# Kernel tuning notes

Measured on AMD Instinct MI355X. Metric: run time of the kernel, lower is better.

Reference implementation:

```python
import jax, jax.numpy as jnp
import numpy as np

N_NODES = 100000
N_EDGES = 1600000
D_IN = 128
D_OUT = 128
EPS = 1e-12  # F.normalize default eps


def setup_inputs() -> dict:
    key = jax.random.key(0)
    k1, k2, k3, k4, k5 = jax.random.split(key, 5)
    x = jax.random.normal(k1, (N_NODES, D_IN), dtype=jnp.float32)
    edge_index = jax.random.randint(k2, (2, N_EDGES), 0, N_NODES, dtype=jnp.int64)
    # PyG SAGEConv params: lin_l (neighbor path, with bias), lin_r (root path, no bias)
    s = 1.0 / np.sqrt(D_IN)
    W_l = jax.random.uniform(k3, (D_IN, D_OUT), jnp.float32, -s, s)
    b_l = jax.random.uniform(k4, (D_OUT,), jnp.float32, -s, s)
    W_r = jax.random.uniform(k5, (D_IN, D_OUT), jnp.float32, -s, s)
    return {"x": x, "edge_index": edge_index, "W_l": W_l, "b_l": b_l, "W_r": W_r}


def reference(x, edge_index, W_l, b_l, W_r):
    n = x.shape[0]
    src = edge_index[0]  # message source nodes (x_j)
    dst = edge_index[1]  # aggregation targets (i)
    # gather + mean scatter-reduce
    msg = x[src]                                            # [E, D_IN]
    summed = jax.ops.segment_sum(msg, dst, num_segments=n)  # [N, D_IN]
    cnt = jax.ops.segment_sum(jnp.ones((msg.shape[0],), x.dtype), dst, num_segments=n)
    mean = summed / jnp.maximum(cnt, 1.0)[:, None]
    # lin_l(mean) + lin_r(x), then row-wise L2 normalize
    out = mean @ W_l + b_l + x @ W_r                        # [N, D_OUT]
    norm = jnp.sqrt(jnp.sum(out * out, axis=-1, keepdims=True))
    return out / jnp.maximum(norm, EPS)
```

## Files before the change

### kernel.cpp

```cpp
#include <hip/hip_runtime.h>
#include <hip/hip_bf16.h>

#define N_NODES 100000
#define N_EDGES 1600000
#define D 128
#define TILES (N_NODES / 16)
#define WPB 8
#define NBKT 196
#define NPB 512
#define EPB 8192
#define PBLK 196

typedef __attribute__((ext_vector_type(4))) float f32x4;
typedef __attribute__((ext_vector_type(2))) float f32x2;
typedef __attribute__((ext_vector_type(8))) short short8;
typedef __attribute__((ext_vector_type(4))) unsigned int u32x4;
typedef __attribute__((ext_vector_type(2))) unsigned int u32x2;

static __device__ __forceinline__ unsigned short f2bf(float f) {
  unsigned u = __float_as_uint(f);
  u += 0x7fffu + ((u >> 16) & 1u);
  return (unsigned short)(u >> 16);
}

static __device__ __forceinline__ void acc4(u32x2 u, float& a0, float& a1,
                                            float& a2, float& a3) {
  a0 += __uint_as_float(u[0] << 16);
  a1 += __uint_as_float(u[0] & 0xffff0000u);
  a2 += __uint_as_float(u[1] << 16);
  a3 += __uint_as_float(u[1] & 0xffff0000u);
}

__global__ __launch_bounds__(256) void cvt_k(const float* __restrict__ x,
                                             unsigned* __restrict__ xh) {
  size_t i = (size_t)blockIdx.x * 256 + threadIdx.x;
  const f32x4* p = (const f32x4*)(x + i * 8);
  f32x4 v0 = p[0], v1 = p[1];
  u32x4 o;
  o[0] = ((unsigned)f2bf(v0[1]) << 16) | f2bf(v0[0]);
  o[1] = ((unsigned)f2bf(v0[3]) << 16) | f2bf(v0[2]);
  o[2] = ((unsigned)f2bf(v1[1]) << 16) | f2bf(v1[0]);
  o[3] = ((unsigned)f2bf(v1[3]) << 16) | f2bf(v1[2]);
  *(u32x4*)(xh + i * 4) = o;
}

__global__ __launch_bounds__(256) void p1_count(const int* __restrict__ ei,
                                                int* __restrict__ gbcnt) {
  __shared__ int bh[256];
  int t = threadIdx.x;
  bh[t] = 0;
  __syncthreads();
  int base = blockIdx.x * EPB;
  int end = min(base + EPB, N_EDGES);
  for (int i = base + t; i < end; i += 256)
    atomicAdd(&bh[ei[N_EDGES + i] >> 9], 1);
  __syncthreads();
  if (t < NBKT && bh[t]) atomicAdd(&gbcnt[t], bh[t]);
}

__global__ __launch_bounds__(256) void p2_scan(const int* __restrict__ gbcnt,
                                               int* __restrict__ bko,
                                               int* __restrict__ btail) {
  __shared__ int s[256];
  int t = threadIdx.x;
  int v = (t < NBKT) ? gbcnt[t] : 0;
  s[t] = v;
  __syncthreads();
  for (int o = 1; o < 256; o <<= 1) {
    int u = (t >= o) ? s[t - o] : 0;
    __syncthreads();
    s[t] += u;
    __syncthreads();
  }
  if (t < NBKT) {
    int ex = s[t] - v;
    bko[t] = ex;
    btail[t] = ex;
  }
  if (t == 0) bko[NBKT] = N_EDGES;
}

__global__ __launch_bounds__(256) void p3_part(const int* __restrict__ ei,
                                               int* __restrict__ btail,
                                               unsigned* __restrict__ part) {
  __shared__ int bh[256], lbase[256], lcur[256];
  int t = threadIdx.x;
  bh[t] = 0;
  lcur[t] = 0;
  __syncthreads();
  int base = blockIdx.x * EPB;
  int end = min(base + EPB, N_EDGES);
  for (int i = base + t; i < end; i += 256)
    atomicAdd(&bh[ei[N_EDGES + i] >> 9], 1);
  __syncthreads();
  if (t < NBKT && bh[t]) lbase[t] = atomicAdd(&btail[t], bh[t]);
  __syncthreads();
  for (int i = base + t; i < end; i += 256) {
    int dst = ei[N_EDGES + i];
    int src = ei[i];
    int b = dst >> 9;
    int idx = atomicAdd(&lcur[b], 1);
    part[lbase[b] + idx] = ((unsigned)(dst & (NPB - 1)) << 17) | (unsigned)src;
  }
}

__global__ __launch_bounds__(512) void p4_build(const unsigned* __restrict__ part,
                                                const int* __restrict__ bko,
                                                int* __restrict__ cnt,
                                                int* __restrict__ ptr,
                                                int* __restrict__ csr) {
  __shared__ int sc[512];
  __shared__ int sw[512];
  int t = threadIdx.x, b = blockIdx.x;
  int beg = bko[b], end = bko[b + 1];
  sc[t] = 0;
  __syncthreads();
  for (int i = beg + t; i < end; i += 512) atomicAdd(&sc[part[i] >> 17], 1);
  __syncthreads();
  int my = sc[t];
  for (int o = 1; o < 512; o <<= 1) {
    int u = (t >= o) ? sc[t - o] : 0;
    __syncthreads();
    sc[t] += u;
    __syncthreads();
  }
  int ex = sc[t] - my;
  int node = b * NPB + t;
  if (node < N_NODES) {
    cnt[node] = my;
    ptr[node] = beg + ex;
  }
  sw[t] = ex;
  __syncthreads();
  for (int i = beg + t; i < end; i += 512) {
    unsigned c = part[i];
    int pos = atomicAdd(&sw[c >> 17], 1);
    csr[beg + pos] = (int)(c & 0x1FFFFu);
  }
}

__global__ __launch_bounds__(256) void gather2_k(const unsigned* __restrict__ xh,
                                                 const int* __restrict__ csr,
                                                 const int* __restrict__ ptr,
                                                 const int* __restrict__ cnt,
                                                 unsigned* __restrict__ mh) {
  int wid = (blockIdx.x * 256 + threadIdx.x) >> 6;
  int lane = threadIdx.x & 63;
  int half = lane >> 5, lh = lane & 31;
  int node = wid * 2 + half;
  if (node >= N_NODES) return;
  int base = ptr[node];
  int deg = cnt[node];
  float a0 = 0.f, a1 = 0.f, a2 = 0.f, a3 = 0.f;
  float b0 = 0.f, b1 = 0.f, b2 = 0.f, b3 = 0.f;
  for (int c = 0; c < deg; c += 32) {
    int rem = deg - c;
    int n = min(32, rem);
    int eidx = (lh < rem) ? csr[base + c + lh] : 0;
    int j = 0;
    for (; j + 3 < n; j += 4) {
      int s0 = __shfl(eidx, j, 32);
      int s1 = __shfl(eidx, j + 1, 32);
      int s2 = __shfl(eidx, j + 2, 32);
      int s3 = __shfl(eidx, j + 3, 32);
      u32x2 u0 = *(const u32x2*)(xh + (size_t)s0 * 64 + lh * 2);
      u32x2 u1 = *(const u32x2*)(xh + (size_t)s1 * 64 + lh * 2);
      u32x2 u2 = *(const u32x2*)(xh + (size_t)s2 * 64 + lh * 2);
      u32x2 u3 = *(const u32x2*)(xh + (size_t)s3 * 64 + lh * 2);
      acc4(u0, a0, a1, a2, a3);
      acc4(u1, b0, b1, b2, b3);
      acc4(u2, a0, a1, a2, a3);
      acc4(u3, b0, b1, b2, b3);
    }
    for (; j < n; j++) {
      int s0 = __shfl(eidx, j, 32);
      u32x2 u0 = *(const u32x2*)(xh + (size_t)s0 * 64 + lh * 2);
      acc4(u0, a0, a1, a2, a3);
    }
  }
  float inv = 1.0f / fmaxf((float)deg, 1.0f);
  a0 = (a0 + b0) * inv;
  a1 = (a1 + b1) * inv;
  a2 = (a2 + b2) * inv;
  a3 = (a3 + b3) * inv;
  u32x2 o;
  o[0] = ((unsigned)f2bf(a1) << 16) | f2bf(a0);
  o[1] = ((unsigned)f2bf(a3) << 16) | f2bf(a2);
  *(u32x2*)(mh + (size_t)node * 64 + lh * 2) = o;
}

template <bool XH>
__global__ __launch_bounds__(256) void gather_k(const float* __restrict__ x,
                                                const unsigned* __restrict__ xh,
                                                const int* __restrict__ csr,
                                                const int* __restrict__ ptr,
                                                const int* __restrict__ cnt,
                                                float* __restrict__ sums) {
  int node = blockIdx.x * 4 + (threadIdx.x >> 6);
  if (node >= N_NODES) return;
  int lane = threadIdx.x & 63;
  int base = ptr[node];
  int deg = cnt[node];
  float a0 = 0.f, a1 = 0.f, b0 = 0.f, b1 = 0.f;
  for (int c = 0; c < deg; c += 64) {
    int n = min(64, deg - c);
    int eidx = (c + lane < deg) ? csr[base + c + lane] : 0;
    int j = 0;
    for (; j + 1 < n; j += 2) {
      int s0 = __shfl(eidx, j);
      int s1 = __shfl(eidx, j + 1);
      if (XH) {
        unsigned u0 = xh[(size_t)s0 * 64 + lane];
        unsigned u1 = xh[(size_t)s1 * 64 + lane];
        a0 += __uint_as_float(u0 << 16);
        a1 += __uint_as_float(u0 & 0xffff0000u);
        b0 += __uint_as_float(u1 << 16);
        b1 += __uint_as_float(u1 & 0xffff0000u);
      } else {
        f32x2 v0 = *(const f32x2*)(x + (size_t)s0 * D + lane * 2);
        f32x2 v1 = *(const f32x2*)(x + (size_t)s1 * D + lane * 2);
        a0 += v0[0]; a1 += v0[1];
        b0 += v1[0]; b1 += v1[1];
      }
    }
    if (j < n) {
      int s0 = __shfl(eidx, j);
      if (XH) {
        unsigned u0 = xh[(size_t)s0 * 64 + lane];
        a0 += __uint_as_float(u0 << 16);
        a1 += __uint_as_float(u0 & 0xffff0000u);
      } else {
        f32x2 v0 = *(const f32x2*)(x + (size_t)s0 * D + lane * 2);
        a0 += v0[0]; a1 += v0[1];
      }
    }
  }
  f32x2 r;
  r[0] = a0 + b0;
  r[1] = a1 + b1;
  *(f32x2*)(sums + (size_t)node * D + lane * 2) = r;
}

template <int AMODE>
__global__ __launch_bounds__(512) void fused_k(
    const float* __restrict__ x, const unsigned* __restrict__ xh,
    const unsigned* __restrict__ mh, const float* __restrict__ Wl,
    const float* __restrict__ bl, const float* __restrict__ Wr,
    const int* __restrict__ cnt, float* __restrict__ out) {
  __shared__ unsigned short Wt[128 * 256];

  int tid = threadIdx.x;
  for (int i = tid; i < 128 * 256; i += 512) {
    int k = i >> 7;
    int c = i & 127;
    float w = (k < 128) ? Wl[k * 128 + c] : Wr[(k - 128) * 128 + c];
    int phys = (k >> 3) ^ (c & 7);
    Wt[c * 256 + (phys << 3) + (k & 7)] = f2bf(w);
  }
  __syncthreads();

  int tile = blockIdx.x * WPB + (tid >> 6);
  if (tile >= TILES) return;
  int lane = tid & 63;
  int c0 = lane & 15;
  int g = lane >> 4;
  int row0 = tile * 16;

  float inv = 1.0f;
  if (AMODE < 2) inv = 1.0f / fmaxf((float)cnt[row0 + c0], 1.0f);

  f32x4 acc[8];
  #pragma unroll
  for (int ct = 0; ct < 8; ct++)
    for (int j = 0; j < 4; j++) acc[ct][j] = 0.0f;

  #pragma unroll
  for (int kf = 0; kf < 8; kf++) {
    int koff = (kf & 3) * 32 + g * 8;
    short8 af;
    if (kf < 4 && AMODE == 2) {
      af = *(const short8*)((const unsigned short*)mh +
                            (size_t)(row0 + c0) * D + koff);
    } else if (kf >= 4 && AMODE >= 1) {
      af = *(const short8*)((const unsigned short*)xh +
                            (size_t)(row0 + c0) * D + koff);
    } else {
      const float* a_src = (kf < 4) ? out : x;
      float s = (kf < 4) ? inv : 1.0f;
      const float* p = a_src + (size_t)(row0 + c0) * D + koff;
      f32x4 v0 = *(const f32x4*)p;
      f32x4 v1 = *(const f32x4*)(p + 4);
      af[0] = (short)f2bf(v0[0] * s);
      af[1] = (short)f2bf(v0[1] * s);
      af[2] = (short)f2bf(v0[2] * s);
      af[3] = (short)f2bf(v0[3] * s);
      af[4] = (short)f2bf(v1[0] * s);
      af[5] = (short)f2bf(v1[1] * s);
      af[6] = (short)f2bf(v1[2] * s);
      af[7] = (short)f2bf(v1[3] * s);
    }
    #pragma unroll
    for (int ct = 0; ct < 8; ct++) {
      int c = ct * 16 + c0;
      short8 bf = *(const short8*)&Wt[c * 256 + ((((kf << 2) + g) ^ (c & 7)) << 3)];
      acc[ct] = __builtin_amdgcn_mfma_f32_16x16x32_bf16(af, bf, acc[ct], 0, 0, 0);
    }
  }

  float ss[4] = {0.f, 0.f, 0.f, 0.f};
  #pragma unroll
  for (int ct = 0; ct < 8; ct++) {
    float bias = bl[ct * 16 + c0];
    #pragma unroll
    for (int j = 0; j < 4; j++) {
      float v = acc[ct][j] + bias;
      acc[ct][j] = v;
      ss[j] += v * v;
    }
  }
  #pragma unroll
  for (int j = 0; j < 4; j++) {
    float s = ss[j];
    s += __shfl_xor(s, 1);
    s += __shfl_xor(s, 2);
    s += __shfl_xor(s, 4);
    s += __shfl_xor(s, 8);
    ss[j] = 1.0f / fmaxf(sqrtf(s), 1e-12f);
  }
  #pragma unroll
  for (int ct = 0; ct < 8; ct++) {
    #pragma unroll
    for (int j = 0; j < 4; j++) {
      out[(size_t)(row0 + g * 4 + j) * D + ct * 16 + c0] = acc[ct][j] * ss[j];
    }
  }
}

extern "C" void kernel_launch(void* const* d_in, const int* in_sizes, int n_in,
                              void* d_out, int out_size, void* d_ws, size_t ws_size,
                              hipStream_t stream) {
  const float* x  = (const float*)d_in[0];
  const int*   ei = (const int*)d_in[1];
  const float* Wl = (const float*)d_in[2];
  const float* bl = (const float*)d_in[3];
  const float* Wr = (const float*)d_in[4];
  float* out = (float*)d_out;

  int* w = (int*)d_ws;
  int* cnt   = w;
  int* ptr   = w + 100000;
  int* gbcnt = w + 200000;
  int* bko   = w + 200256;
  int* btail = w + 200520;
  unsigned* part = (unsigned*)(w + 200800);
  int* csr   = w + 1800800;
  const size_t XH_OFF = 3400800ULL * 4;
  const size_t MH_OFF = XH_OFF + (size_t)N_NODES * D * 2;
  unsigned* xh = (unsigned*)((char*)d_ws + XH_OFF);
  unsigned* mh = (unsigned*)((char*)d_ws + MH_OFF);
  bool use_xh = ws_size >= MH_OFF;
  bool use_mh = ws_size >= MH_OFF + (size_t)N_NODES * D * 2;

  hipMemsetAsync(gbcnt, 0, 256 * sizeof(int), stream);
  if (use_xh) cvt_k<<<6250, 256, 0, stream>>>(x, xh);
  p1_count<<<PBLK, 256, 0, stream>>>(ei, gbcnt);
  p2_scan<<<1, 256, 0, stream>>>(gbcnt, bko, btail);
  p3_part<<<PBLK, 256, 0, stream>>>(ei, btail, part);
  p4_build<<<NBKT, 512, 0, stream>>>(part, bko, cnt, ptr, csr);

  if (use_mh) {
    gather2_k<<<12500, 256, 0, stream>>>(xh, csr, ptr, cnt, mh);
    fused_k<2><<<(TILES + WPB - 1) / WPB, 512, 0, stream>>>(x, xh, mh, Wl, bl, Wr, cnt, out);
  } else if (use_xh) {
    gather_k<true><<<(N_NODES + 3) / 4, 256, 0, stream>>>(x, xh, csr, ptr, cnt, out);
    fused_k<1><<<(TILES + WPB - 1) / WPB, 512, 0, stream>>>(x, xh, mh, Wl, bl, Wr, cnt, out);
  } else {
    gather_k<false><<<(N_NODES + 3) / 4, 256, 0, stream>>>(x, xh, csr, ptr, cnt, out);
    fused_k<0><<<(TILES + WPB - 1) / WPB, 512, 0, stream>>>(x, xh, mh, Wl, bl, Wr, cnt, out);
  }
}
```

Before: 160.6 us.

## Merge preprocessing kernels, persistent fused GEMM, deeper gather unroll, drop fallbacks

The bf16 conversion and bucket count now run as one launch. The scan kernel is removed: each consumer block recomputes the bucket prefix from the counts, and btail is zeroed by a memset and offset by the recomputed prefix. The gather loop is unrolled to 8 loads in flight, and the fused GEMM becomes a persistent grid of 391 blocks that loads the weights into LDS once and loops over tiles. This cuts launches and redundant weight staging, at the cost of duplicated scan work per block and dropping the small-workspace fallback paths.

```diff
diff --git a/kernel.cpp b/kernel.cpp
--- a/kernel.cpp
+++ b/kernel.cpp
@@ -6,10 +6,12 @@
 #define D 128
 #define TILES (N_NODES / 16)
 #define WPB 8
+#define FBLK 391
 #define NBKT 196
 #define NPB 512
 #define EPB 8192
 #define PBLK 196
+#define CVTB 6250
 
 typedef __attribute__((ext_vector_type(4))) float f32x4;
 typedef __attribute__((ext_vector_type(2))) float f32x2;
@@ -31,69 +33,59 @@
   a3 += __uint_as_float(u[1] & 0xffff0000u);
 }
 
-__global__ __launch_bounds__(256) void cvt_k(const float* __restrict__ x,
-                                             unsigned* __restrict__ xh) {
-  size_t i = (size_t)blockIdx.x * 256 + threadIdx.x;
-  const f32x4* p = (const f32x4*)(x + i * 8);
-  f32x4 v0 = p[0], v1 = p[1];
-  u32x4 o;
-  o[0] = ((unsigned)f2bf(v0[1]) << 16) | f2bf(v0[0]);
-  o[1] = ((unsigned)f2bf(v0[3]) << 16) | f2bf(v0[2]);
-  o[2] = ((unsigned)f2bf(v1[1]) << 16) | f2bf(v1[0]);
-  o[3] = ((unsigned)f2bf(v1[3]) << 16) | f2bf(v1[2]);
-  *(u32x4*)(xh + i * 4) = o;
-}
-
-__global__ __launch_bounds__(256) void p1_count(const int* __restrict__ ei,
-                                                int* __restrict__ gbcnt) {
+__global__ __launch_bounds__(256) void cvtp1_k(const float* __restrict__ x,
+                                               unsigned* __restrict__ xh,
+                                               const int* __restrict__ ei,
+                                               int* __restrict__ gbcnt) {
   __shared__ int bh[256];
+  if (blockIdx.x < CVTB) {
+    size_t i = (size_t)blockIdx.x * 256 + threadIdx.x;
+    const f32x4* p = (const f32x4*)(x + i * 8);
+    f32x4 v0 = p[0], v1 = p[1];
+    u32x4 o;
+    o[0] = ((unsigned)f2bf(v0[1]) << 16) | f2bf(v0[0]);
+    o[1] = ((unsigned)f2bf(v0[3]) << 16) | f2bf(v0[2]);
+    o[2] = ((unsigned)f2bf(v1[1]) << 16) | f2bf(v1[0]);
+    o[3] = ((unsigned)f2bf(v1[3]) << 16) | f2bf(v1[2]);
+    *(u32x4*)(xh + i * 4) = o;
+    return;
+  }
   int t = threadIdx.x;
   bh[t] = 0;
+  __syncthreads();
+  int base = (blockIdx.x - CVTB) * EPB;
+  int end = min(base + EPB, N_EDGES);
+  for (int i = base + t; i < end; i += 256)
+    atomicAdd(&bh[ei[N_EDGES + i] >> 9], 1);
+  __syncthreads();
+  if (t < NBKT && bh[t]) atomicAdd(&gbcnt[t], bh[t]);
+}
+
+__global__ __launch_bounds__(256) void p3_part(const int* __restrict__ ei,
+                                               const int* __restrict__ gbcnt,
+                                               int* __restrict__ btail,
+                                               unsigned* __restrict__ part) {
+  __shared__ int sb[256], bh[256], lbase[256], lcur[256];
+  int t = threadIdx.x;
+  int v = (t < NBKT) ? gbcnt[t] : 0;
+  sb[t] = v;
+  __syncthreads();
+  for (int o = 1; o < 256; o <<= 1) {
+    int u = (t >= o) ? sb[t - o] : 0;
+    __syncthreads();
+    sb[t] += u;
+    __syncthreads();
+  }
+  int myex = sb[t] - v;
+  bh[t] = 0;
+  lcur[t] = 0;
   __syncthreads();
   int base = blockIdx.x * EPB;
   int end = min(base + EPB, N_EDGES);
   for (int i = base + t; i < end; i += 256)
     atomicAdd(&bh[ei[N_EDGES + i] >> 9], 1);
   __syncthreads();
-  if (t < NBKT && bh[t]) atomicAdd(&gbcnt[t], bh[t]);
-}
-
-__global__ __launch_bounds__(256) void p2_scan(const int* __restrict__ gbcnt,
-                                               int* __restrict__ bko,
-                                               int* __restrict__ btail) {
-  __shared__ int s[256];
-  int t = threadIdx.x;
-  int v = (t < NBKT) ? gbcnt[t] : 0;
-  s[t] = v;
-  __syncthreads();
-  for (int o = 1; o < 256; o <<= 1) {
-    int u = (t >= o) ? s[t - o] : 0;
-    __syncthreads();
-    s[t] += u;
-    __syncthreads();
-  }
-  if (t < NBKT) {
-    int ex = s[t] - v;
-    bko[t] = ex;
-    btail[t] = ex;
-  }
-  if (t == 0) bko[NBKT] = N_EDGES;
-}
-
-__global__ __launch_bounds__(256) void p3_part(const int* __restrict__ ei,
-                                               int* __restrict__ btail,
-                                               unsigned* __restrict__ part) {
-  __shared__ int bh[256], lbase[256], lcur[256];
-  int t = threadIdx.x;
-  bh[t] = 0;
-  lcur[t] = 0;
-  __syncthreads();
-  int base = blockIdx.x * EPB;
-  int end = min(base + EPB, N_EDGES);
-  for (int i = base + t; i < end; i += 256)
-    atomicAdd(&bh[ei[N_EDGES + i] >> 9], 1);
-  __syncthreads();
-  if (t < NBKT && bh[t]) lbase[t] = atomicAdd(&btail[t], bh[t]);
+  if (t < NBKT && bh[t]) lbase[t] = myex + atomicAdd(&btail[t], bh[t]);
   __syncthreads();
   for (int i = base + t; i < end; i += 256) {
     int dst = ei[N_EDGES + i];
@@ -105,16 +97,30 @@
 }
 
 __global__ __launch_bounds__(512) void p4_build(const unsigned* __restrict__ part,
-                                                const int* __restrict__ bko,
+                                                const int* __restrict__ gbcnt,
                                                 int* __restrict__ cnt,
                                                 int* __restrict__ ptr,
                                                 int* __restrict__ csr) {
   __shared__ int sc[512];
   __shared__ int sw[512];
+  __shared__ int s_beg, s_end;
   int t = threadIdx.x, b = blockIdx.x;
-  int beg = bko[b], end = bko[b + 1];
+  if (t < 256) sw[t] = (t < NBKT) ? gbcnt[t] : 0;
+  __syncthreads();
+  for (int o = 1; o < 256; o <<= 1) {
+    int u = (t >= o && t < 256) ? sw[t - o] : 0;
+    __syncthreads();
+    if (t < 256) sw[t] += u;
+    __syncthreads();
+  }
+  if (t == 0) {
+    int g = gbcnt[b];
+    s_end = sw[b];
+    s_beg = sw[b] - g;
+  }
   sc[t] = 0;
   __syncthreads();
+  int beg = s_beg, end = s_end;
   for (int i = beg + t; i < end; i += 512) atomicAdd(&sc[part[i] >> 17], 1);
   __syncthreads();
   int my = sc[t];
@@ -158,6 +164,32 @@
     int n = min(32, rem);
     int eidx = (lh < rem) ? csr[base + c + lh] : 0;
     int j = 0;
+    for (; j + 7 < n; j += 8) {
+      int s0 = __shfl(eidx, j, 32);
+      int s1 = __shfl(eidx, j + 1, 32);
+      int s2 = __shfl(eidx, j + 2, 32);
+      int s3 = __shfl(eidx, j + 3, 32);
+      int s4 = __shfl(eidx, j + 4, 32);
+      int s5 = __shfl(eidx, j + 5, 32);
+      int s6 = __shfl(eidx, j + 6, 32);
+      int s7 = __shfl(eidx, j + 7, 32);
+      u32x2 u0 = *(const u32x2*)(xh + (size_t)s0 * 64 + lh * 2);
+      u32x2 u1 = *(const u32x2*)(xh + (size_t)s1 * 64 + lh * 2);
+      u32x2 u2 = *(const u32x2*)(xh + (size_t)s2 * 64 + lh * 2);
+      u32x2 u3 = *(const u32x2*)(xh + (size_t)s3 * 64 + lh * 2);
+      u32x2 u4 = *(const u32x2*)(xh + (size_t)s4 * 64 + lh * 2);
+      u32x2 u5 = *(const u32x2*)(xh + (size_t)s5 * 64 + lh * 2);
+      u32x2 u6 = *(const u32x2*)(xh + (size_t)s6 * 64 + lh * 2);
+      u32x2 u7 = *(const u32x2*)(xh + (size_t)s7 * 64 + lh * 2);
+      acc4(u0, a0, a1, a2, a3);
+      acc4(u1, b0, b1, b2, b3);
+      acc4(u2, a0, a1, a2, a3);
+      acc4(u3, b0, b1, b2, b3);
+      acc4(u4, a0, a1, a2, a3);
+      acc4(u5, b0, b1, b2, b3);
+      acc4(u6, a0, a1, a2, a3);
+      acc4(u7, b0, b1, b2, b3);
+    }
     for (; j + 3 < n; j += 4) {
       int s0 = __shfl(eidx, j, 32);
       int s1 = __shfl(eidx, j + 1, 32);
@@ -189,64 +221,10 @@
   *(u32x2*)(mh + (size_t)node * 64 + lh * 2) = o;
 }
 
-template <bool XH>
-__global__ __launch_bounds__(256) void gather_k(const float* __restrict__ x,
-                                                const unsigned* __restrict__ xh,
-                                                const int* __restrict__ csr,
-                                                const int* __restrict__ ptr,
-                                                const int* __restrict__ cnt,
-                                                float* __restrict__ sums) {
-  int node = blockIdx.x * 4 + (threadIdx.x >> 6);
-  if (node >= N_NODES) return;
-  int lane = threadIdx.x & 63;
-  int base = ptr[node];
-  int deg = cnt[node];
-  float a0 = 0.f, a1 = 0.f, b0 = 0.f, b1 = 0.f;
-  for (int c = 0; c < deg; c += 64) {
-    int n = min(64, deg - c);
-    int eidx = (c + lane < deg) ? csr[base + c + lane] : 0;
-    int j = 0;
-    for (; j + 1 < n; j += 2) {
-      int s0 = __shfl(eidx, j);
-      int s1 = __shfl(eidx, j + 1);
-      if (XH) {
-        unsigned u0 = xh[(size_t)s0 * 64 + lane];
-        unsigned u1 = xh[(size_t)s1 * 64 + lane];
-        a0 += __uint_as_float(u0 << 16);
-        a1 += __uint_as_float(u0 & 0xffff0000u);
-        b0 += __uint_as_float(u1 << 16);
-        b1 += __uint_as_float(u1 & 0xffff0000u);
-      } else {
-        f32x2 v0 = *(const f32x2*)(x + (size_t)s0 * D + lane * 2);
-        f32x2 v1 = *(const f32x2*)(x + (size_t)s1 * D + lane * 2);
-        a0 += v0[0]; a1 += v0[1];
-        b0 += v1[0]; b1 += v1[1];
-      }
-    }
-    if (j < n) {
-      int s0 = __shfl(eidx, j);
-      if (XH) {
-        unsigned u0 = xh[(size_t)s0 * 64 + lane];
-        a0 += __uint_as_float(u0 << 16);
-        a1 += __uint_as_float(u0 & 0xffff0000u);
-      } else {
-        f32x2 v0 = *(const f32x2*)(x + (size_t)s0 * D + lane * 2);
-        a0 += v0[0]; a1 += v0[1];
-      }
-    }
-  }
-  f32x2 r;
-  r[0] = a0 + b0;
-  r[1] = a1 + b1;
-  *(f32x2*)(sums + (size_t)node * D + lane * 2) = r;
-}
-
-template <int AMODE>
 __global__ __launch_bounds__(512) void fused_k(
-    const float* __restrict__ x, const unsigned* __restrict__ xh,
-    const unsigned* __restrict__ mh, const float* __restrict__ Wl,
-    const float* __restrict__ bl, const float* __restrict__ Wr,
-    const int* __restrict__ cnt, float* __restrict__ out) {
+    const unsigned* __restrict__ xh, const unsigned* __restrict__ mh,
+    const float* __restrict__ Wl, const float* __restrict__ bl,
+    const float* __restrict__ Wr, float* __restrict__ out) {
   __shared__ unsigned short Wt[128 * 256];
 
   int tid = threadIdx.x;
@@ -259,79 +237,59 @@
   }
   __syncthreads();
 
-  int tile = blockIdx.x * WPB + (tid >> 6);
-  if (tile >= TILES) return;
   int lane = tid & 63;
+  int wid = tid >> 6;
   int c0 = lane & 15;
   int g = lane >> 4;
-  int row0 = tile * 16;
-
-  float inv = 1.0f;
-  if (AMODE < 2) inv = 1.0f / fmaxf((float)cnt[row0 + c0], 1.0f);
-
-  f32x4 acc[8];
-  #pragma unroll
-  for (int ct = 0; ct < 8; ct++)
-    for (int j = 0; j < 4; j++) acc[ct][j] = 0.0f;
-
-  #pragma unroll
-  for (int kf = 0; kf < 8; kf++) {
-    int koff = (kf & 3) * 32 + g * 8;
-    short8 af;
-    if (kf < 4 && AMODE == 2) {
-      af = *(const short8*)((const unsigned short*)mh +
-                            (size_t)(row0 + c0) * D + koff);
-    } else if (kf >= 4 && AMODE >= 1) {
-      af = *(const short8*)((const unsigned short*)xh +
-                            (size_t)(row0 + c0) * D + koff);
-    } else {
-      const float* a_src = (kf < 4) ? out : x;
-      float s = (kf < 4) ? inv : 1.0f;
-      const float* p = a_src + (size_t)(row0 + c0) * D + koff;
-      f32x4 v0 = *(const f32x4*)p;
-      f32x4 v1 = *(const f32x4*)(p + 4);
-      af[0] = (short)f2bf(v0[0] * s);
-      af[1] = (short)f2bf(v0[1] * s);
-      af[2] = (short)f2bf(v0[2] * s);
-      af[3] = (short)f2bf(v0[3] * s);
-      af[4] = (short)f2bf(v1[0] * s);
-      af[5] = (short)f2bf(v1[1] * s);
-      af[6] = (short)f2bf(v1[2] * s);
-      af[7] = (short)f2bf(v1[3] * s);
-    }
+
+  for (int tile = blockIdx.x * WPB + wid; tile < TILES; tile += FBLK * WPB) {
+    int row0 = tile * 16;
+
+    f32x4 acc[8];
+    #pragma unroll
+    for (int ct = 0; ct < 8; ct++)
+      for (int j = 0; j < 4; j++) acc[ct][j] = 0.0f;
+
+    #pragma unroll
+    for (int kf = 0; kf < 8; kf++) {
+      int koff = (kf & 3) * 32 + g * 8;
+      const unsigned short* a_src =
+          (const unsigned short*)((kf < 4) ? mh : xh);
+      short8 af = *(const short8*)(a_src + (size_t)(row0 + c0) * D + koff);
+      #pragma unroll
+      for (int ct = 0; ct < 8; ct++) {
+        int c = ct * 16 + c0;
+        short8 bf = *(const short8*)&Wt[c * 256 + ((((kf << 2) + g) ^ (c & 7)) << 3)];
+        acc[ct] = __builtin_amdgcn_mfma_f32_16x16x32_bf16(af, bf, acc[ct], 0, 0, 0);
+      }
+    }
+
+    float ss[4] = {0.f, 0.f, 0.f, 0.f};
     #pragma unroll
     for (int ct = 0; ct < 8; ct++) {
-      int c = ct * 16 + c0;
-      short8 bf = *(const short8*)&Wt[c * 256 + ((((kf << 2) + g) ^ (c & 7)) << 3)];
-      acc[ct] = __builtin_amdgcn_mfma_f32_16x16x32_bf16(af, bf, acc[ct], 0, 0, 0);
-    }
-  }
-
-  float ss[4] = {0.f, 0.f, 0.f, 0.f};
-  #pragma unroll
-  for (int ct = 0; ct < 8; ct++) {
-    float bias = bl[ct * 16 + c0];
+      float bias = bl[ct * 16 + c0];
+      #pragma unroll
+      for (int j = 0; j < 4; j++) {
+        float v = acc[ct][j] + bias;
+        acc[ct][j] = v;
+        ss[j] += v * v;
+      }
+    }
     #pragma unroll
     for (int j = 0; j < 4; j++) {
-      float v = acc[ct][j] + bias;
-      acc[ct][j] = v;
-      ss[j] += v * v;
-    }
-  }
-  #pragma unroll
-  for (int j = 0; j < 4; j++) {
-    float s = ss[j];
-    s += __shfl_xor(s, 1);
-    s += __shfl_xor(s, 2);
-    s += __shfl_xor(s, 4);
-    s += __shfl_xor(s, 8);
-    ss[j] = 1.0f / fmaxf(sqrtf(s), 1e-12f);
-  }
-  #pragma unroll
-  for (int ct = 0; ct < 8; ct++) {
-    #pragma unroll
-    for (int j = 0; j < 4; j++) {
-      out[(size_t)(row0 + g * 4 + j) * D + ct * 16 + c0] = acc[ct][j] * ss[j];
+      float s = ss[j];
+      s += __shfl_xor(s, 1);
+      s += __shfl_xor(s, 2);
+      s += __shfl_xor(s, 4);
+      s += __shfl_xor(s, 8);
+      ss[j] = 1.0f / fmaxf(sqrtf(s), 1e-12f);
+    }
+    #pragma unroll
+    for (int ct = 0; ct < 8; ct++) {
+      #pragma unroll
+      for (int j = 0; j < 4; j++) {
+        out[(size_t)(row0 + g * 4 + j) * D + ct * 16 + c0] = acc[ct][j] * ss[j];
+      }
     }
   }
 }
@@ -350,32 +308,18 @@
   int* cnt   = w;
   int* ptr   = w + 100000;
   int* gbcnt = w + 200000;
-  int* bko   = w + 200256;
-  int* btail = w + 200520;
-  unsigned* part = (unsigned*)(w + 200800);
-  int* csr   = w + 1800800;
-  const size_t XH_OFF = 3400800ULL * 4;
+  int* btail = w + 200256;
+  unsigned* part = (unsigned*)(w + 200512);
+  int* csr   = w + 1800512;
+  const size_t XH_OFF = 3400512ULL * 4;
   const size_t MH_OFF = XH_OFF + (size_t)N_NODES * D * 2;
   unsigned* xh = (unsigned*)((char*)d_ws + XH_OFF);
   unsigned* mh = (unsigned*)((char*)d_ws + MH_OFF);
-  bool use_xh = ws_size >= MH_OFF;
-  bool use_mh = ws_size >= MH_OFF + (size_t)N_NODES * D * 2;
-
-  hipMemsetAsync(gbcnt, 0, 256 * sizeof(int), stream);
-  if (use_xh) cvt_k<<<6250, 256, 0, stream>>>(x, xh);
-  p1_count<<<PBLK, 256, 0, stream>>>(ei, gbcnt);
-  p2_scan<<<1, 256, 0, stream>>>(gbcnt, bko, btail);
-  p3_part<<<PBLK, 256, 0, stream>>>(ei, btail, part);
-  p4_build<<<NBKT, 512, 0, stream>>>(part, bko, cnt, ptr, csr);
-
-  if (use_mh) {
-    gather2_k<<<12500, 256, 0, stream>>>(xh, csr, ptr, cnt, mh);
-    fused_k<2><<<(TILES + WPB - 1) / WPB, 512, 0, stream>>>(x, xh, mh, Wl, bl, Wr, cnt, out);
-  } else if (use_xh) {
-    gather_k<true><<<(N_NODES + 3) / 4, 256, 0, stream>>>(x, xh, csr, ptr, cnt, out);
-    fused_k<1><<<(TILES + WPB - 1) / WPB, 512, 0, stream>>>(x, xh, mh, Wl, bl, Wr, cnt, out);
-  } else {
-    gather_k<false><<<(N_NODES + 3) / 4, 256, 0, stream>>>(x, xh, csr, ptr, cnt, out);
-    fused_k<0><<<(TILES + WPB - 1) / WPB, 512, 0, stream>>>(x, xh, mh, Wl, bl, Wr, cnt, out);
-  }
-}
+
+  hipMemsetAsync(gbcnt, 0, 512 * sizeof(int), stream);
+  cvtp1_k<<<CVTB + PBLK, 256, 0, stream>>>(x, xh, ei, gbcnt);
+  p3_part<<<PBLK, 256, 0, stream>>>(ei, gbcnt, btail, part);
+  p4_build<<<NBKT, 512, 0, stream>>>(part, gbcnt, cnt, ptr, csr);
+  gather2_k<<<12500, 256, 0, stream>>>(xh, csr, ptr, cnt, mh);
+  fused_k<<<FBLK, 512, 0, stream>>>(xh, mh, Wl, bl, Wr, out);
+}
```

After: 200.1 us. +24.6%, slower.
